# Performance work log

Measured on AMD Instinct MI355X. Metric: run time of the kernel, lower is better.

The kernel has to match this reference:

```python
import jax, jax.numpy as jnp
import numpy as np

N, E = 50000, 400000
FN, FE, FG = 32, 16, 16
H1, H2 = 256, 128


def seg_mean(x, idx, n):
    # mean of edge rows per segment; empty segments -> 0 (scatter_mean semantics)
    s = jax.ops.segment_sum(x, idx, num_segments=n)
    c = jax.ops.segment_sum(jnp.ones((x.shape[0], 1), x.dtype), idx, num_segments=n)
    return s / jnp.maximum(c, 1.0)


def setup_inputs() -> dict:
    key = jax.random.key(0)
    ks = jax.random.split(key, 32)
    g = lambda k, shape, s=0.05: jax.random.normal(k, shape, dtype=jnp.float32) * s
    return {
        'nodes': g(ks[0], (N, FN), 1.0),
        'edges': g(ks[1], (E, FE), 1.0),
        'globals_u': g(ks[2], (FG,), 1.0),
        'senders': jax.random.randint(ks[3], (E,), 0, N, dtype=jnp.int32),
        'receivers': jax.random.randint(ks[4], (E,), 0, N, dtype=jnp.int32),
        'We1': g(ks[5], (FE, H1)), 'be1': jnp.zeros((H1,), jnp.float32),
        'Wn1': g(ks[6], (FN, H1)), 'Win1': g(ks[7], (H1, H1)), 'Wout1': g(ks[8], (H1, H1)), 'bn1': jnp.zeros((H1,), jnp.float32),
        'Wu1': g(ks[9], (FG, H1)), 'Wgn1': g(ks[10], (H1, H1)), 'Wge1': g(ks[11], (H1, H1)), 'bu1': jnp.zeros((H1,), jnp.float32),
        'We2': g(ks[12], (H1, H2)), 'be2': jnp.zeros((H2,), jnp.float32),
        'Wn2': g(ks[13], (H1, H2)), 'Win2': g(ks[14], (H2, H2)), 'Wout2': g(ks[15], (H2, H2)), 'bn2': jnp.zeros((H2,), jnp.float32),
        'Wu2': g(ks[16], (H1, H2)), 'Wgn2': g(ks[17], (H2, H2)), 'Wge2': g(ks[18], (H2, H2)), 'bu2': jnp.zeros((H2,), jnp.float32),
    }


def reference(nodes, edges, globals_u, senders, receivers,
              We1, be1, Wn1, Win1, Wout1, bn1, Wu1, Wgn1, Wge1, bu1,
              We2, be2, Wn2, Win2, Wout2, bn2, Wu2, Wgn2, Wge2, bu2):
    n = nodes.shape[0]
    # --- block 1 (width 256) ---
    e1 = jax.nn.relu(edges @ We1 + be1)                                  # [E, H1]
    inc1 = seg_mean(e1, receivers, n)                                    # avg incoming edges per node
    out1 = seg_mean(e1, senders, n)                                      # avg outgoing edges per node
    n1 = jax.nn.relu(nodes @ Wn1 + inc1 @ Win1 + out1 @ Wout1 + bn1)     # [N, H1]
    u1 = jax.nn.relu(globals_u @ Wu1 + n1.mean(0) @ Wgn1 + e1.mean(0) @ Wge1 + bu1)  # [H1]
    # --- block 2 (width 128) ---
    e2 = jax.nn.relu(e1 @ We2 + be2)                                     # [E, H2]
    inc2 = seg_mean(e2, receivers, n)
    out2 = seg_mean(e2, senders, n)
    n2 = jax.nn.relu(n1 @ Wn2 + inc2 @ Win2 + out2 @ Wout2 + bn2)        # [N, H2]
    u2 = jax.nn.relu(u1 @ Wu2 + n2.mean(0) @ Wgn2 + e2.mean(0) @ Wge2 + bu2)  # [H2]
    return n2, e2, u2
```

## Files before the change

kernel.cpp:

```cpp
#include <hip/hip_runtime.h>
#include <hip/hip_bf16.h>
#include <stdint.h>

#define NN 50000
#define NE 400000
#define FN 32
#define FE 16
#define FG 16
#define H1 256
#define H2 128
#define M2 (2*NN)
#define SCAN_B 391
#define LCAP 1536

typedef unsigned short u16;
typedef __bf16 bfv8 __attribute__((ext_vector_type(8)));
typedef float f32v4 __attribute__((ext_vector_type(4)));
typedef u16 usv2 __attribute__((ext_vector_type(2)));
typedef u16 usv4 __attribute__((ext_vector_type(4)));
typedef u16 usv8 __attribute__((ext_vector_type(8)));

#define APK 264
#define AP2 136
#define EP1 40

__device__ __forceinline__ u16 f2b(float x){
  __hip_bfloat16 h = __float2bfloat16(x);
  return *reinterpret_cast<u16*>(&h);
}
__device__ __forceinline__ float bf2f(u16 u){
  union{uint32_t i; float f;} v; v.i = ((uint32_t)u) << 16; return v.f;
}

template<int NCK, int NNT, int PITCH>
__device__ __forceinline__ void gemm_tiles(const u16* a_s, const u16* __restrict__ pB,
                                           int w, int l, f32v4* acc)
{
  const int lr = l & 15, q = l >> 4;
  const bfv8* bp = (const bfv8*)pB;
  for (int ck = 0; ck < NCK; ck++){
    bfv8 a = *(const bfv8*)&a_s[(w*16 + lr)*PITCH + ck*32 + q*8];
    #pragma unroll
    for (int nt = 0; nt < NNT; nt++){
      bfv8 b = bp[(ck*NNT + nt)*64 + l];
      acc[nt] = __builtin_amdgcn_mfma_f32_16x16x32_bf16(a, b, acc[nt], 0, 0, 0);
    }
  }
}

template<int C4PR_LOG2>
__device__ __forceinline__ void stage_rows(u16* a_s, const float* __restrict__ src,
                                           long n0, int t)
{
  const int c4pr = 1 << C4PR_LOG2;
  for (int idx = t; idx < 64*c4pr; idx += 256){
    int row = idx >> C4PR_LOG2, c4 = idx & (c4pr - 1);
    long n = n0 + row;
    float x0=0.f, x1=0.f, x2=0.f, x3=0.f;
    if (n < NN){
      const float4 v = *(const float4*)&src[(n << (C4PR_LOG2 + 2)) + c4*4];
      x0 = v.x; x1 = v.y; x2 = v.z; x3 = v.w;
    }
    usv4 o; o.x = f2b(x0); o.y = f2b(x1); o.z = f2b(x2); o.w = f2b(x3);
    *(usv4*)&a_s[row*APK + c4*4] = o;
  }
}

struct PD { const float* src; u16* dst; int K, N, Ks; };
struct PackArgs { PD d[8]; };

__global__ __launch_bounds__(64) void pack_weights(PackArgs A){
  int b = blockIdx.x, l = threadIdx.x;
  int mi = 0, base = 0;
  for (; mi < 8; mi++){
    int tiles = (A.d[mi].K >> 5) * (A.d[mi].N >> 4);
    if (b < base + tiles) break;
    base += tiles;
  }
  const PD d = A.d[mi];
  const int tile = b - base;
  const int ntn = d.N >> 4;
  const int ck = tile / ntn, nt = tile % ntn;
  const int lr = l & 15, q = l >> 4;
  const int col = nt*16 + lr;
  usv8 o;
  #pragma unroll
  for (int j = 0; j < 8; j++){
    int k = ck*32 + q*8 + j;
    o[j] = (k < d.Ks) ? f2b(d.src[(long)k * d.N + col]) : (u16)0;
  }
  *(usv8*)&d.dst[((long)tile*64 + l)*8] = o;
}

__global__ __launch_bounds__(256) void csr_count(const int* __restrict__ recv,
    const int* __restrict__ send, int* cnt, int* pos_in, int* pos_out)
{
  int e = blockIdx.x*256 + threadIdx.x;
  if (e >= NE) return;
  pos_in [e] = atomicAdd(&cnt[recv[e]], 1);
  pos_out[e] = atomicAdd(&cnt[NN + send[e]], 1);
}

__global__ __launch_bounds__(256) void scan_blocks(const int* __restrict__ cnt,
    int* off, int* btot)
{
  __shared__ int s[256];
  int b = blockIdx.x, t = threadIdx.x;
  int i = b*256 + t;
  int v = (i < M2) ? cnt[i] : 0;
  s[t] = v; __syncthreads();
  int acc = v;
  for (int d = 1; d < 256; d <<= 1){
    int add = (t >= d) ? s[t-d] : 0;
    __syncthreads();
    acc += add; s[t] = acc;
    __syncthreads();
  }
  if (i < M2) off[i] = acc - v;
  if (t == 255) btot[b] = acc;
}

__global__ __launch_bounds__(256) void scan_tops(int* btot){
  __shared__ int s[512], ts[256];
  int t = threadIdx.x;
  s[t]     = (t < SCAN_B) ? btot[t] : 0;
  s[256+t] = (256+t < SCAN_B) ? btot[256+t] : 0;
  __syncthreads();
  int a0 = s[2*t], a1 = s[2*t+1];
  int tot = a0 + a1;
  ts[t] = tot; __syncthreads();
  int acc = tot;
  for (int d = 1; d < 256; d <<= 1){
    int add = (t >= d) ? ts[t-d] : 0;
    __syncthreads();
    acc += add; ts[t] = acc;
    __syncthreads();
  }
  int excl = acc - tot;
  if (2*t   < SCAN_B) btot[2*t]   = excl;
  if (2*t+1 < SCAN_B) btot[2*t+1] = excl + a0;
}

__global__ __launch_bounds__(256) void scan_fix(int* off, const int* __restrict__ btot){
  int i = blockIdx.x*256 + threadIdx.x;
  if (i < M2) off[i] += btot[blockIdx.x];
}

__global__ __launch_bounds__(256) void csr_fill(const int* __restrict__ recv,
    const int* __restrict__ send, const int* __restrict__ off,
    const int* __restrict__ pos_in, const int* __restrict__ pos_out, int* lis)
{
  int e = blockIdx.x*256 + threadIdx.x;
  if (e >= NE) return;
  lis[off[recv[e]]      + pos_in [e]] = e;
  lis[off[NN + send[e]] + pos_out[e]] = e;
}

__global__ __launch_bounds__(256) void edge1_kernel(const float* __restrict__ edges,
    const u16* __restrict__ pWe1, const float* __restrict__ be1,
    u16* __restrict__ e1b, float* __restrict__ e1_cs)
{
  __shared__ __align__(16) u16 a_es[64*EP1];
  __shared__ float cs_s[H1];
  const int t = threadIdx.x;
  const long e0 = (long)blockIdx.x * 64;
  const int w = t >> 6, l = t & 63, lr = l & 15, q = l >> 4;
  cs_s[t] = 0.f;
  {
    int row = t >> 2, c4 = t & 3;
    float4 v = *(const float4*)&edges[(e0 + row)*FE + c4*4];
    usv4 o = { f2b(v.x), f2b(v.y), f2b(v.z), f2b(v.w) };
    *(usv4*)&a_es[row*EP1 + c4*4] = o;
    *(usv4*)&a_es[row*EP1 + 16 + c4*4] = (usv4){0,0,0,0};
  }
  __syncthreads();
  f32v4 acc[16];
  #pragma unroll
  for (int nt = 0; nt < 16; nt++) acc[nt] = (f32v4){0.f,0.f,0.f,0.f};
  gemm_tiles<1,16,EP1>(a_es, pWe1, w, l, acc);

  #pragma unroll
  for (int nt = 0; nt < 16; nt++){
    const int j = nt*16 + lr;
    const float b = be1[j];
    float part = 0.f;
    #pragma unroll
    for (int r = 0; r < 4; r++){
      const int m = w*16 + q*4 + r;
      float v = fmaxf(acc[nt][r] + b, 0.f);
      e1b[(e0 + m)*H1 + j] = f2b(v);
      part += v;
    }
    atomicAdd(&cs_s[j], part);
  }
  __syncthreads();
  atomicAdd(&e1_cs[t], cs_s[t]);
}

__global__ __launch_bounds__(256) void e2_kernel(float* __restrict__ e2f,
    const u16* __restrict__ pWe2, const float* __restrict__ be2, float* __restrict__ e2_cs)
{
  __shared__ __align__(16) u16 a_s[64*APK];
  __shared__ float cs_s[H2];
  const int t = threadIdx.x;
  const long e0 = (long)blockIdx.x * 64;
  const int w = t >> 6, l = t & 63, lr = l & 15, q = l >> 4;
  if (t < H2) cs_s[t] = 0.f;
  const u16* e1u = (const u16*)e2f;
  for (int idx = t; idx < 64*32; idx += 256){
    int row = idx >> 5, ch = idx & 31;
    usv8 v = *(const usv8*)&e1u[(e0 + row)*H1 + ch*8];
    *(usv8*)&a_s[row*APK + ch*8] = v;
  }
  __syncthreads();
  f32v4 acc[8];
  #pragma unroll
  for (int nt = 0; nt < 8; nt++) acc[nt] = (f32v4){0.f,0.f,0.f,0.f};
  gemm_tiles<8,8,APK>(a_s, pWe2, w, l, acc);

  #pragma unroll
  for (int nt = 0; nt < 8; nt++){
    const int j = nt*16 + lr;
    const float b = be2[j];
    float part = 0.f;
    #pragma unroll
    for (int r = 0; r < 4; r++){
      const int m = w*16 + q*4 + r;
      float v = fmaxf(acc[nt][r] + b, 0.f);
      e2f[(e0 + m)*H2 + j] = v;
      part += v;
    }
    atomicAdd(&cs_s[j], part);
  }
  __syncthreads();
  if (t < H2) atomicAdd(&e2_cs[t], cs_s[t]);
}

template<int PITCH>
__device__ __forceinline__ void gather_h1(u16* a_s, const u16* __restrict__ src,
    const int* lst, const int* roff, int base, const int* __restrict__ lis_g, int w, int l)
{
  for (int rr = 0; rr < 16; rr++){
    int r = w + rr*4;
    int rs = roff[r] - base, re = roff[r+1] - base;
    float s0=0.f, s1=0.f, s2=0.f, s3=0.f;
    int j = rs;
    if (re <= LCAP){
      for (; j + 4 <= re; j += 4){
        int eA = lst[j], eB = lst[j+1], eC = lst[j+2], eD = lst[j+3];
        usv4 a = *(const usv4*)&src[(long)eA*H1 + l*4];
        usv4 b = *(const usv4*)&src[(long)eB*H1 + l*4];
        usv4 c = *(const usv4*)&src[(long)eC*H1 + l*4];
        usv4 d = *(const usv4*)&src[(long)eD*H1 + l*4];
        s0 += (bf2f(a.x)+bf2f(b.x)) + (bf2f(c.x)+bf2f(d.x));
        s1 += (bf2f(a.y)+bf2f(b.y)) + (bf2f(c.y)+bf2f(d.y));
        s2 += (bf2f(a.z)+bf2f(b.z)) + (bf2f(c.z)+bf2f(d.z));
        s3 += (bf2f(a.w)+bf2f(b.w)) + (bf2f(c.w)+bf2f(d.w));
      }
      if (j + 2 <= re){
        int eA = lst[j], eB = lst[j+1]; j += 2;
        usv4 a = *(const usv4*)&src[(long)eA*H1 + l*4];
        usv4 b = *(const usv4*)&src[(long)eB*H1 + l*4];
        s0 += bf2f(a.x)+bf2f(b.x); s1 += bf2f(a.y)+bf2f(b.y);
        s2 += bf2f(a.z)+bf2f(b.z); s3 += bf2f(a.w)+bf2f(b.w);
      }
      if (j < re){
        int eA = lst[j];
        usv4 a = *(const usv4*)&src[(long)eA*H1 + l*4];
        s0 += bf2f(a.x); s1 += bf2f(a.y); s2 += bf2f(a.z); s3 += bf2f(a.w);
      }
    } else {
      for (; j < re; ++j){
        int eA = (j < LCAP) ? lst[j] : lis_g[base + j];
        usv4 a = *(const usv4*)&src[(long)eA*H1 + l*4];
        s0 += bf2f(a.x); s1 += bf2f(a.y); s2 += bf2f(a.z); s3 += bf2f(a.w);
      }
    }
    float rd = 1.f / fmaxf((float)(re - rs), 1.f);
    usv4 o = { f2b(s0*rd), f2b(s1*rd), f2b(s2*rd), f2b(s3*rd) };
    *(usv4*)&a_s[r*PITCH + l*4] = o;
  }
}

template<int PITCH>
__device__ __forceinline__ void gather_h2(u16* a_s, const float* __restrict__ src,
    const int* lst, const int* roff, int base, const int* __restrict__ lis_g, int w, int l)
{
  for (int rr = 0; rr < 16; rr++){
    int r = w + rr*4;
    int rs = roff[r] - base, re = roff[r+1] - base;
    float s0=0.f, s1=0.f;
    int j = rs;
    if (re <= LCAP){
      for (; j + 4 <= re; j += 4){
        int eA = lst[j], eB = lst[j+1], eC = lst[j+2], eD = lst[j+3];
        float2 a = *(const float2*)&src[(long)eA*H2 + l*2];
        float2 b = *(const float2*)&src[(long)eB*H2 + l*2];
        float2 c = *(const float2*)&src[(long)eC*H2 + l*2];
        float2 d = *(const float2*)&src[(long)eD*H2 + l*2];
        s0 += (a.x+b.x) + (c.x+d.x);
        s1 += (a.y+b.y) + (c.y+d.y);
      }
      if (j + 2 <= re){
        int eA = lst[j], eB = lst[j+1]; j += 2;
        float2 a = *(const float2*)&src[(long)eA*H2 + l*2];
        float2 b = *(const float2*)&src[(long)eB*H2 + l*2];
        s0 += a.x + b.x; s1 += a.y + b.y;
      }
      if (j < re){
        int eA = lst[j];
        float2 a = *(const float2*)&src[(long)eA*H2 + l*2];
        s0 += a.x; s1 += a.y;
      }
    } else {
      for (; j < re; ++j){
        int eA = (j < LCAP) ? lst[j] : lis_g[base + j];
        float2 a = *(const float2*)&src[(long)eA*H2 + l*2];
        s0 += a.x; s1 += a.y;
      }
    }
    float rd = 1.f / fmaxf((float)(re - rs), 1.f);
    usv2 o = { f2b(s0*rd), f2b(s1*rd) };
    *(usv2*)&a_s[r*PITCH + l*2] = o;
  }
}

__global__ __launch_bounds__(256, 3) void node1_kernel(
    const float* __restrict__ nodes, const u16* __restrict__ e1b,
    const int* __restrict__ off, const int* __restrict__ lis,
    const u16* __restrict__ pWn1, const u16* __restrict__ pWin1, const u16* __restrict__ pWout1,
    const float* __restrict__ bn1, u16* __restrict__ n1b, float* __restrict__ n1_cs)
{
  __shared__ __align__(16) u16 a_s[64*APK];
  __shared__ int ilA[LCAP], ilB[LCAP];
  __shared__ int roff[65], roff2[65];
  __shared__ float cs_s[H1];
  const int t = threadIdx.x;
  const long n0 = (long)blockIdx.x * 64;
  const int w = t >> 6, l = t & 63, lr = l & 15, q = l >> 4;

  cs_s[t] = 0.f;
  if (t <= 64){
    long idx = n0 + t;
    roff [t] = (idx >= NN) ? NE     : off[idx];
    roff2[t] = (idx >= NN) ? 2*NE   : off[NN + idx];
  }
  __syncthreads();
  const int inb = roff[0],  in_total  = roff[64]  - inb;
  const int onb = roff2[0], out_total = roff2[64] - onb;
  for (int j = t; j < in_total  && j < LCAP; j += 256) ilA[j] = lis[inb + j];
  for (int j = t; j < out_total && j < LCAP; j += 256) ilB[j] = lis[onb + j];
  __syncthreads();

  f32v4 acc[16];
  #pragma unroll
  for (int nt = 0; nt < 16; nt++) acc[nt] = (f32v4){0.f,0.f,0.f,0.f};

  gather_h1<APK>(a_s, e1b, ilA, roff, inb, lis, w, l);
  __syncthreads();
  gemm_tiles<8,16,APK>(a_s, pWin1, w, l, acc);
  __syncthreads();

  gather_h1<APK>(a_s, e1b, ilB, roff2, onb, lis, w, l);
  __syncthreads();
  gemm_tiles<8,16,APK>(a_s, pWout1, w, l, acc);
  __syncthreads();

  stage_rows<3>(a_s, nodes, n0, t);
  __syncthreads();
  gemm_tiles<1,16,APK>(a_s, pWn1, w, l, acc);

  #pragma unroll
  for (int nt = 0; nt < 16; nt++){
    const int j = nt*16 + lr;
    const float b = bn1[j];
    float part = 0.f;
    #pragma unroll
    for (int r = 0; r < 4; r++){
      const int row = w*16 + q*4 + r;
      const long n = n0 + row;
      if (n < NN){
        float v = fmaxf(acc[nt][r] + b, 0.f);
        n1b[n*H1 + j] = f2b(v);
        part += v;
      }
    }
    atomicAdd(&cs_s[j], part);
  }
  __syncthreads();
  atomicAdd(&n1_cs[t], cs_s[t]);
}

__global__ __launch_bounds__(256, 4) void node2_kernel(
    const u16* __restrict__ n1b, const float* __restrict__ e2f,
    const int* __restrict__ off, const int* __restrict__ lis,
    const u16* __restrict__ pWn2, const u16* __restrict__ pWin2, const u16* __restrict__ pWout2,
    const float* __restrict__ bn2, float* __restrict__ n2_out, float* __restrict__ n2_cs)
{
  __shared__ __align__(16) u16 a_s[64*AP2];
  __shared__ int ilA[LCAP], ilB[LCAP];
  __shared__ int roff[65], roff2[65];
  __shared__ float cs_s[H2];
  const int t = threadIdx.x;
  const long n0 = (long)blockIdx.x * 64;
  const int w = t >> 6, l = t & 63, lr = l & 15, q = l >> 4;

  if (t < H2) cs_s[t] = 0.f;
  if (t <= 64){
    long idx = n0 + t;
    roff [t] = (idx >= NN) ? NE     : off[idx];
    roff2[t] = (idx >= NN) ? 2*NE   : off[NN + idx];
  }
  __syncthreads();
  const int inb = roff[0],  in_total  = roff[64]  - inb;
  const int onb = roff2[0], out_total = roff2[64] - onb;
  for (int j = t; j < in_total  && j < LCAP; j += 256) ilA[j] = lis[inb + j];
  for (int j = t; j < out_total && j < LCAP; j += 256) ilB[j] = lis[onb + j];
  __syncthreads();

  f32v4 acc[8];
  #pragma unroll
  for (int nt = 0; nt < 8; nt++) acc[nt] = (f32v4){0.f,0.f,0.f,0.f};

  for (int h = 0; h < 2; h++){
    for (int idx = t; idx < 64*16; idx += 256){
      int row = idx >> 4, ch = idx & 15;
      long n = n0 + row;
      usv8 v = (usv8){0,0,0,0,0,0,0,0};
      if (n < NN) v = *(const usv8*)&n1b[n*H1 + h*128 + ch*8];
      *(usv8*)&a_s[row*AP2 + ch*8] = v;
    }
    __syncthreads();
    gemm_tiles<4,8,AP2>(a_s, pWn2 + h*(4*8*64*8), w, l, acc);
    __syncthreads();
  }

  gather_h2<AP2>(a_s, e2f, ilA, roff, inb, lis, w, l);
  __syncthreads();
  gemm_tiles<4,8,AP2>(a_s, pWin2, w, l, acc);
  __syncthreads();

  gather_h2<AP2>(a_s, e2f, ilB, roff2, onb, lis, w, l);
  __syncthreads();
  gemm_tiles<4,8,AP2>(a_s, pWout2, w, l, acc);

  #pragma unroll
  for (int nt = 0; nt < 8; nt++){
    const int j = nt*16 + lr;
    const float b = bn2[j];
    float part = 0.f;
    #pragma unroll
    for (int r = 0; r < 4; r++){
      const int row = w*16 + q*4 + r;
      const long n = n0 + row;
      if (n < NN){
        float v = fmaxf(acc[nt][r] + b, 0.f);
        n2_out[n*H2 + j] = v;
        part += v;
      }
    }
    atomicAdd(&cs_s[j], part);
  }
  __syncthreads();
  if (t < H2) atomicAdd(&n2_cs[t], cs_s[t]);
}

__global__ void u1_kernel(const float* __restrict__ gu, const float* __restrict__ Wu1,
    const float* __restrict__ Wgn1, const float* __restrict__ Wge1, const float* __restrict__ bu1,
    const float* __restrict__ n1_cs, const float* __restrict__ e1_cs, float* __restrict__ u1v)
{
    const int j = threadIdx.x;
    float acc = bu1[j];
    #pragma unroll
    for (int k = 0; k < FG; k++) acc += gu[k] * Wu1[k*H1 + j];
    for (int k = 0; k < H1; k++) acc += (n1_cs[k] * (1.f/NN)) * Wgn1[k*H1 + j];
    for (int k = 0; k < H1; k++) acc += (e1_cs[k] * (1.f/NE)) * Wge1[k*H1 + j];
    u1v[j] = fmaxf(acc, 0.f);
}

__global__ void u2_kernel(const float* __restrict__ u1v, const float* __restrict__ Wu2,
    const float* __restrict__ Wgn2, const float* __restrict__ Wge2, const float* __restrict__ bu2,
    const float* __restrict__ n2_cs, const float* __restrict__ e2_cs, float* __restrict__ u2_out)
{
    const int j = threadIdx.x;
    float acc = bu2[j];
    for (int k = 0; k < H1; k++) acc += u1v[k] * Wu2[k*H2 + j];
    for (int k = 0; k < H2; k++) acc += (n2_cs[k] * (1.f/NN)) * Wgn2[k*H2 + j];
    for (int k = 0; k < H2; k++) acc += (e2_cs[k] * (1.f/NE)) * Wge2[k*H2 + j];
    u2_out[j] = fmaxf(acc, 0.f);
}

extern "C" void kernel_launch(void* const* d_in, const int* in_sizes, int n_in,
                              void* d_out, int out_size, void* d_ws, size_t ws_size,
                              hipStream_t stream)
{
    (void)in_sizes; (void)n_in; (void)out_size; (void)ws_size;
    const float* nodes = (const float*)d_in[0];
    const float* edges = (const float*)d_in[1];
    const float* gu    = (const float*)d_in[2];
    const int* senders   = (const int*)d_in[3];
    const int* receivers = (const int*)d_in[4];
    const float* We1  = (const float*)d_in[5];  const float* be1 = (const float*)d_in[6];
    const float* Wn1  = (const float*)d_in[7];  const float* Win1= (const float*)d_in[8];
    const float* Wout1= (const float*)d_in[9];  const float* bn1 = (const float*)d_in[10];
    const float* Wu1  = (const float*)d_in[11]; const float* Wgn1= (const float*)d_in[12];
    const float* Wge1 = (const float*)d_in[13]; const float* bu1 = (const float*)d_in[14];
    const float* We2  = (const float*)d_in[15]; const float* be2 = (const float*)d_in[16];
    const float* Wn2  = (const float*)d_in[17]; const float* Win2= (const float*)d_in[18];
    const float* Wout2= (const float*)d_in[19]; const float* bn2 = (const float*)d_in[20];
    const float* Wu2  = (const float*)d_in[21]; const float* Wgn2= (const float*)d_in[22];
    const float* Wge2 = (const float*)d_in[23]; const float* bu2 = (const float*)d_in[24];

    float* ws = (float*)d_ws;
    size_t o = 0;
    int*   cnt    = (int*)(ws + o);  o += M2;
    float* e1_cs  = ws + o;          o += 256;
    float* n1_cs  = ws + o;          o += 256;
    float* e2_cs  = ws + o;          o += 128;
    float* n2_cs  = ws + o;          o += 128;
    const size_t zero_bytes = o * sizeof(float);
    float* u1v    = ws + o;          o += 256;
    int*   off    = (int*)(ws + o);  o += M2;
    int*   pos_in = (int*)(ws + o);  o += NE;
    int*   pos_out= (int*)(ws + o);  o += NE;
    int*   lis    = (int*)(ws + o);  o += 2*NE;
    int*   btot   = (int*)(ws + o);  o += 400;

    u16* pbase = (u16*)(ws + o);
    size_t po = 0;
    u16* pWin1 = pbase + po;  po += (size_t)H1*H1;
    u16* pWout1= pbase + po;  po += (size_t)H1*H1;
    u16* pWn1  = pbase + po;  po += (size_t)FN*H1;
    u16* pWe1  = pbase + po;  po += (size_t)32*H1;
    u16* pWe2  = pbase + po;  po += (size_t)H1*H2;
    u16* pWn2  = pbase + po;  po += (size_t)H1*H2;
    u16* pWin2 = pbase + po;  po += (size_t)H2*H2;
    u16* pWout2= pbase + po;  po += (size_t)H2*H2;
    o += (po + 1) / 2;

    u16* n1b = (u16*)(ws + o);

    float* n2_out = (float*)d_out;
    float* e2f    = n2_out + (size_t)NN*H2;
    float* u2_out = n2_out + (size_t)(NN + NE)*H2;
    u16*   e1b    = (u16*)e2f;

    hipMemsetAsync(d_ws, 0, zero_bytes, stream);

    PackArgs pa;
    pa.d[0] = {Win1,  pWin1,  H1, H1, H1};
    pa.d[1] = {Wout1, pWout1, H1, H1, H1};
    pa.d[2] = {Wn1,   pWn1,   FN, H1, FN};
    pa.d[3] = {We1,   pWe1,   32, H1, FE};
    pa.d[4] = {We2,   pWe2,   H1, H2, H1};
    pa.d[5] = {Wn2,   pWn2,   H1, H2, H1};
    pa.d[6] = {Win2,  pWin2,  H2, H2, H2};
    pa.d[7] = {Wout2, pWout2, H2, H2, H2};
    int total_tiles = 0;
    for (int i = 0; i < 8; i++) total_tiles += (pa.d[i].K >> 5) * (pa.d[i].N >> 4);
    pack_weights<<<total_tiles, 64, 0, stream>>>(pa);

    const int EG = (NE + 255)/256;
    csr_count<<<EG, 256, 0, stream>>>(receivers, senders, cnt, pos_in, pos_out);
    scan_blocks<<<SCAN_B, 256, 0, stream>>>(cnt, off, btot);
    scan_tops<<<1, 256, 0, stream>>>(btot);
    scan_fix<<<SCAN_B, 256, 0, stream>>>(off, btot);
    csr_fill<<<EG, 256, 0, stream>>>(receivers, senders, off, pos_in, pos_out, lis);

    edge1_kernel<<<NE/64, 256, 0, stream>>>(edges, pWe1, be1, e1b, e1_cs);

    node1_kernel<<<(NN + 63)/64, 256, 0, stream>>>(nodes, e1b, off, lis,
        pWn1, pWin1, pWout1, bn1, n1b, n1_cs);

    u1_kernel<<<1, H1, 0, stream>>>(gu, Wu1, Wgn1, Wge1, bu1, n1_cs, e1_cs, u1v);

    e2_kernel<<<NE/64, 256, 0, stream>>>(e2f, pWe2, be2, e2_cs);

    node2_kernel<<<(NN + 63)/64, 256, 0, stream>>>(n1b, e2f, off, lis,
        pWn2, pWin2, pWout2, bn2, n2_out, n2_cs);

    u2_kernel<<<1, H2, 0, stream>>>(u1v, Wu2, Wgn2, Wge2, bu2, n2_cs, e2_cs, u2_out);
}
```

Measured before the change: 1.044 ms.

## Vectorize epilogue stores via permuted column layout and partition column-sum atomics

```diff
diff --git a/kernel.cpp b/kernel.cpp
--- a/kernel.cpp
+++ b/kernel.cpp
@@ -12,6 +12,7 @@
 #define M2 (2*NN)
 #define SCAN_B 391
 #define LCAP 1536
+#define NPART 256
 
 typedef unsigned short u16;
 typedef __bf16 bfv8 __attribute__((ext_vector_type(8)));
@@ -23,6 +24,7 @@
 #define APK 264
 #define AP2 136
 #define EP1 40
+
 
 __device__ __forceinline__ u16 f2b(float x){
   __hip_bfloat16 h = __float2bfloat16(x);
@@ -66,7 +68,7 @@
   }
 }
 
-struct PD { const float* src; u16* dst; int K, N, Ks; };
+struct PD { const float* src; u16* dst; int K, N, Ks, perm; };
 struct PackArgs { PD d[8]; };
 
 __global__ __launch_bounds__(64) void pack_weights(PackArgs A){
@@ -87,7 +89,8 @@
   #pragma unroll
   for (int j = 0; j < 8; j++){
     int k = ck*32 + q*8 + j;
-    o[j] = (k < d.Ks) ? f2b(d.src[(long)k * d.N + col]) : (u16)0;
+    int sk = (d.perm == 1) ? (((k & 15) << 4) | (k >> 4)) : k;
+    o[j] = (k < d.Ks) ? f2b(d.src[(long)sk * d.N + col]) : (u16)0;
   }
   *(usv8*)&d.dst[((long)tile*64 + l)*8] = o;
 }
@@ -158,14 +161,16 @@
 
 __global__ __launch_bounds__(256) void edge1_kernel(const float* __restrict__ edges,
     const u16* __restrict__ pWe1, const float* __restrict__ be1,
-    u16* __restrict__ e1b, float* __restrict__ e1_cs)
+    u16* __restrict__ e1b, float* __restrict__ e1p)
 {
   __shared__ __align__(16) u16 a_es[64*EP1];
   __shared__ float cs_s[H1];
+  __shared__ float bs[H1];
   const int t = threadIdx.x;
   const long e0 = (long)blockIdx.x * 64;
   const int w = t >> 6, l = t & 63, lr = l & 15, q = l >> 4;
   cs_s[t] = 0.f;
+  bs[t] = be1[t];
   {
     int row = t >> 2, c4 = t & 3;
     float4 v = *(const float4*)&edges[(e0 + row)*FE + c4*4];
@@ -181,31 +186,38 @@
 
   #pragma unroll
   for (int nt = 0; nt < 16; nt++){
-    const int j = nt*16 + lr;
-    const float b = be1[j];
+    const float b = bs[nt*16 + lr];
     float part = 0.f;
     #pragma unroll
     for (int r = 0; r < 4; r++){
-      const int m = w*16 + q*4 + r;
       float v = fmaxf(acc[nt][r] + b, 0.f);
-      e1b[(e0 + m)*H1 + j] = f2b(v);
-      part += v;
-    }
-    atomicAdd(&cs_s[j], part);
-  }
-  __syncthreads();
-  atomicAdd(&e1_cs[t], cs_s[t]);
+      acc[nt][r] = v; part += v;
+    }
+    atomicAdd(&cs_s[nt*16 + lr], part);
+  }
+  #pragma unroll
+  for (int r = 0; r < 4; r++){
+    const int m = w*16 + q*4 + r;
+    usv8 o0, o1;
+    #pragma unroll
+    for (int h = 0; h < 8; h++){ o0[h] = f2b(acc[h][r]); o1[h] = f2b(acc[8+h][r]); }
+    *(usv8*)&e1b[(e0 + m)*H1 + lr*16]     = o0;
+    *(usv8*)&e1b[(e0 + m)*H1 + lr*16 + 8] = o1;
+  }
+  __syncthreads();
+  atomicAdd(&e1p[(blockIdx.x & (NPART-1))*H1 + t], cs_s[t]);
 }
 
 __global__ __launch_bounds__(256) void e2_kernel(float* __restrict__ e2f,
-    const u16* __restrict__ pWe2, const float* __restrict__ be2, float* __restrict__ e2_cs)
+    const u16* __restrict__ pWe2, const float* __restrict__ be2, float* __restrict__ e2p)
 {
   __shared__ __align__(16) u16 a_s[64*APK];
   __shared__ float cs_s[H2];
+  __shared__ float bs[H2];
   const int t = threadIdx.x;
   const long e0 = (long)blockIdx.x * 64;
   const int w = t >> 6, l = t & 63, lr = l & 15, q = l >> 4;
-  if (t < H2) cs_s[t] = 0.f;
+  if (t < H2){ cs_s[t] = 0.f; bs[t] = be2[t]; }
   const u16* e1u = (const u16*)e2f;
   for (int idx = t; idx < 64*32; idx += 256){
     int row = idx >> 5, ch = idx & 31;
@@ -220,20 +232,37 @@
 
   #pragma unroll
   for (int nt = 0; nt < 8; nt++){
-    const int j = nt*16 + lr;
-    const float b = be2[j];
+    const float b = bs[nt*16 + lr];
     float part = 0.f;
     #pragma unroll
     for (int r = 0; r < 4; r++){
-      const int m = w*16 + q*4 + r;
       float v = fmaxf(acc[nt][r] + b, 0.f);
-      e2f[(e0 + m)*H2 + j] = v;
-      part += v;
-    }
-    atomicAdd(&cs_s[j], part);
-  }
-  __syncthreads();
-  if (t < H2) atomicAdd(&e2_cs[t], cs_s[t]);
+      acc[nt][r] = v; part += v;
+    }
+    atomicAdd(&cs_s[nt*16 + lr], part);
+  }
+  __syncthreads();
+  float* fl = (float*)a_s;
+  #pragma unroll
+  for (int r = 0; r < 4; r++){
+    const int m = w*16 + q*4 + r;
+    const int sw = (m & 7) * 4;
+    #pragma unroll
+    for (int nt = 0; nt < 8; nt++)
+      fl[m*128 + ((nt*16 + lr) ^ sw)] = acc[nt][r];
+  }
+  __syncthreads();
+  {
+    const int row = t >> 2, c = t & 3;
+    const int sw = (row & 7) * 4;
+    #pragma unroll
+    for (int k = 0; k < 8; k++){
+      const int wi = (c*32 + k*4) ^ sw;
+      float4 v = *(const float4*)&fl[row*128 + wi];
+      *(float4*)&e2f[(e0 + row)*H2 + c*32 + k*4] = v;
+    }
+  }
+  if (t < H2) atomicAdd(&e2p[(blockIdx.x & (NPART-1))*H2 + t], cs_s[t]);
 }
 
 template<int PITCH>
@@ -329,17 +358,19 @@
     const float* __restrict__ nodes, const u16* __restrict__ e1b,
     const int* __restrict__ off, const int* __restrict__ lis,
     const u16* __restrict__ pWn1, const u16* __restrict__ pWin1, const u16* __restrict__ pWout1,
-    const float* __restrict__ bn1, u16* __restrict__ n1b, float* __restrict__ n1_cs)
+    const float* __restrict__ bn1, u16* __restrict__ n1b, float* __restrict__ n1p)
 {
   __shared__ __align__(16) u16 a_s[64*APK];
   __shared__ int ilA[LCAP], ilB[LCAP];
   __shared__ int roff[65], roff2[65];
   __shared__ float cs_s[H1];
+  __shared__ float bs[H1];
   const int t = threadIdx.x;
   const long n0 = (long)blockIdx.x * 64;
   const int w = t >> 6, l = t & 63, lr = l & 15, q = l >> 4;
 
   cs_s[t] = 0.f;
+  bs[t] = bn1[t];
   if (t <= 64){
     long idx = n0 + t;
     roff [t] = (idx >= NN) ? NE     : off[idx];
@@ -372,30 +403,38 @@
 
   #pragma unroll
   for (int nt = 0; nt < 16; nt++){
-    const int j = nt*16 + lr;
-    const float b = bn1[j];
+    const float b = bs[nt*16 + lr];
     float part = 0.f;
     #pragma unroll
     for (int r = 0; r < 4; r++){
-      const int row = w*16 + q*4 + r;
-      const long n = n0 + row;
-      if (n < NN){
-        float v = fmaxf(acc[nt][r] + b, 0.f);
-        n1b[n*H1 + j] = f2b(v);
-        part += v;
-      }
-    }
-    atomicAdd(&cs_s[j], part);
-  }
-  __syncthreads();
-  atomicAdd(&n1_cs[t], cs_s[t]);
+      const long n = n0 + w*16 + q*4 + r;
+      float v = fmaxf(acc[nt][r] + b, 0.f);
+      acc[nt][r] = v;
+      if (n < NN) part += v;
+    }
+    atomicAdd(&cs_s[nt*16 + lr], part);
+  }
+  #pragma unroll
+  for (int r = 0; r < 4; r++){
+    const int m = w*16 + q*4 + r;
+    const long n = n0 + m;
+    if (n < NN){
+      usv8 o0, o1;
+      #pragma unroll
+      for (int h = 0; h < 8; h++){ o0[h] = f2b(acc[h][r]); o1[h] = f2b(acc[8+h][r]); }
+      *(usv8*)&n1b[n*H1 + lr*16]     = o0;
+      *(usv8*)&n1b[n*H1 + lr*16 + 8] = o1;
+    }
+  }
+  __syncthreads();
+  atomicAdd(&n1p[(blockIdx.x & (NPART-1))*H1 + t], cs_s[t]);
 }
 
 __global__ __launch_bounds__(256, 4) void node2_kernel(
     const u16* __restrict__ n1b, const float* __restrict__ e2f,
     const int* __restrict__ off, const int* __restrict__ lis,
     const u16* __restrict__ pWn2, const u16* __restrict__ pWin2, const u16* __restrict__ pWout2,
-    const float* __restrict__ bn2, float* __restrict__ n2_out, float* __restrict__ n2_cs)
+    const float* __restrict__ bn2, float* __restrict__ n2_out, float* __restrict__ n2p)
 {
   __shared__ __align__(16) u16 a_s[64*AP2];
   __shared__ int ilA[LCAP], ilB[LCAP];
@@ -462,31 +501,43 @@
     atomicAdd(&cs_s[j], part);
   }
   __syncthreads();
-  if (t < H2) atomicAdd(&n2_cs[t], cs_s[t]);
+  if (t < H2) atomicAdd(&n2p[(blockIdx.x & (NPART-1))*H2 + t], cs_s[t]);
 }
 
 __global__ void u1_kernel(const float* __restrict__ gu, const float* __restrict__ Wu1,
     const float* __restrict__ Wgn1, const float* __restrict__ Wge1, const float* __restrict__ bu1,
-    const float* __restrict__ n1_cs, const float* __restrict__ e1_cs, float* __restrict__ u1v)
-{
+    const float* __restrict__ n1p, const float* __restrict__ e1p, float* __restrict__ u1v)
+{
+    __shared__ float ncs[H1], ecs[H1];
     const int j = threadIdx.x;
+    float sn = 0.f, se = 0.f;
+    #pragma unroll 8
+    for (int c = 0; c < NPART; c++){ sn += n1p[c*H1 + j]; se += e1p[c*H1 + j]; }
+    ncs[j] = sn; ecs[j] = se;
+    __syncthreads();
     float acc = bu1[j];
     #pragma unroll
     for (int k = 0; k < FG; k++) acc += gu[k] * Wu1[k*H1 + j];
-    for (int k = 0; k < H1; k++) acc += (n1_cs[k] * (1.f/NN)) * Wgn1[k*H1 + j];
-    for (int k = 0; k < H1; k++) acc += (e1_cs[k] * (1.f/NE)) * Wge1[k*H1 + j];
+    for (int k = 0; k < H1; k++) acc += (ncs[k] * (1.f/NN)) * Wgn1[k*H1 + j];
+    for (int k = 0; k < H1; k++) acc += (ecs[k] * (1.f/NE)) * Wge1[k*H1 + j];
     u1v[j] = fmaxf(acc, 0.f);
 }
 
 __global__ void u2_kernel(const float* __restrict__ u1v, const float* __restrict__ Wu2,
     const float* __restrict__ Wgn2, const float* __restrict__ Wge2, const float* __restrict__ bu2,
-    const float* __restrict__ n2_cs, const float* __restrict__ e2_cs, float* __restrict__ u2_out)
-{
+    const float* __restrict__ n2p, const float* __restrict__ e2p, float* __restrict__ u2_out)
+{
+    __shared__ float ncs[H2], ecs[H2];
     const int j = threadIdx.x;
+    float sn = 0.f, se = 0.f;
+    #pragma unroll 8
+    for (int c = 0; c < NPART; c++){ sn += n2p[c*H2 + j]; se += e2p[c*H2 + j]; }
+    ncs[j] = sn; ecs[j] = se;
+    __syncthreads();
     float acc = bu2[j];
     for (int k = 0; k < H1; k++) acc += u1v[k] * Wu2[k*H2 + j];
-    for (int k = 0; k < H2; k++) acc += (n2_cs[k] * (1.f/NN)) * Wgn2[k*H2 + j];
-    for (int k = 0; k < H2; k++) acc += (e2_cs[k] * (1.f/NE)) * Wge2[k*H2 + j];
+    for (int k = 0; k < H2; k++) acc += (ncs[k] * (1.f/NN)) * Wgn2[k*H2 + j];
+    for (int k = 0; k < H2; k++) acc += (ecs[k] * (1.f/NE)) * Wge2[k*H2 + j];
     u2_out[j] = fmaxf(acc, 0.f);
 }
 
@@ -514,10 +565,10 @@
     float* ws = (float*)d_ws;
     size_t o = 0;
     int*   cnt    = (int*)(ws + o);  o += M2;
-    float* e1_cs  = ws + o;          o += 256;
-    float* n1_cs  = ws + o;          o += 256;
-    float* e2_cs  = ws + o;          o += 128;
-    float* n2_cs  = ws + o;          o += 128;
+    float* e1p    = ws + o;          o += (size_t)NPART*H1;
+    float* n1p    = ws + o;          o += (size_t)NPART*H1;
+    float* e2p    = ws + o;          o += (size_t)NPART*H2;
+    float* n2p    = ws + o;          o += (size_t)NPART*H2;
     const size_t zero_bytes = o * sizeof(float);
     float* u1v    = ws + o;          o += 256;
     int*   off    = (int*)(ws + o);  o += M2;
@@ -548,14 +599,14 @@
     hipMemsetAsync(d_ws, 0, zero_bytes, stream);
 
     PackArgs pa;
-    pa.d[0] = {Win1,  pWin1,  H1, H1, H1};
-    pa.d[1] = {Wout1, pWout1, H1, H1, H1};
-    pa.d[2] = {Wn1,   pWn1,   FN, H1, FN};
-    pa.d[3] = {We1,   pWe1,   32, H1, FE};
-    pa.d[4] = {We2,   pWe2,   H1, H2, H1};
-    pa.d[5] = {Wn2,   pWn2,   H1, H2, H1};
-    pa.d[6] = {Win2,  pWin2,  H2, H2, H2};
-    pa.d[7] = {Wout2, pWout2, H2, H2, H2};
+    pa.d[0] = {Win1,  pWin1,  H1, H1, H1, 1};
+    pa.d[1] = {Wout1, pWout1, H1, H1, H1, 1};
+    pa.d[2] = {Wn1,   pWn1,   FN, H1, FN, 0};
+    pa.d[3] = {We1,   pWe1,   32, H1, FE, 0};
+    pa.d[4] = {We2,   pWe2,   H1, H2, H1, 1};
+    pa.d[5] = {Wn2,   pWn2,   H1, H2, H1, 1};
+    pa.d[6] = {Win2,  pWin2,  H2, H2, H2, 0};
+    pa.d[7] = {Wout2, pWout2, H2, H2, H2, 0};
     int total_tiles = 0;
     for (int i = 0; i < 8; i++) total_tiles += (pa.d[i].K >> 5) * (pa.d[i].N >> 4);
     pack_weights<<<total_tiles, 64, 0, stream>>>(pa);
@@ -567,17 +618,17 @@
     scan_fix<<<SCAN_B, 256, 0, stream>>>(off, btot);
     csr_fill<<<EG, 256, 0, stream>>>(receivers, senders, off, pos_in, pos_out, lis);
 
-    edge1_kernel<<<NE/64, 256, 0, stream>>>(edges, pWe1, be1, e1b, e1_cs);
+    edge1_kernel<<<NE/64, 256, 0, stream>>>(edges, pWe1, be1, e1b, e1p);
 
     node1_kernel<<<(NN + 63)/64, 256, 0, stream>>>(nodes, e1b, off, lis,
-        pWn1, pWin1, pWout1, bn1, n1b, n1_cs);
-
-    u1_kernel<<<1, H1, 0, stream>>>(gu, Wu1, Wgn1, Wge1, bu1, n1_cs, e1_cs, u1v);
-
-    e2_kernel<<<NE/64, 256, 0, stream>>>(e2f, pWe2, be2, e2_cs);
+        pWn1, pWin1, pWout1, bn1, n1b, n1p);
+
+    u1_kernel<<<1, H1, 0, stream>>>(gu, Wu1, Wgn1, Wge1, bu1, n1p, e1p, u1v);
+
+    e2_kernel<<<NE/64, 256, 0, stream>>>(e2f, pWe2, be2, e2p);
 
     node2_kernel<<<(NN + 63)/64, 256, 0, stream>>>(n1b, e2f, off, lis,
-        pWn2, pWin2, pWout2, bn2, n2_out, n2_cs);
-
-    u2_kernel<<<1, H2, 0, stream>>>(u1v, Wu2, Wgn2, Wge2, bu2, n2_cs, e2_cs, u2_out);
-}
+        pWn2, pWin2, pWout2, bn2, n2_out, n2p);
+
+    u2_kernel<<<1, H2, 0, stream>>>(u1v, Wu2, Wgn2, Wge2, bu2, n2p, e2p, u2_out);
+}
```

New measurement: 1.012 ms. 3.1% less time.
